# Kernel tuning notes

Hardware: AMD Instinct MI355X
Metric: run time of the kernel (lower is better)

The kernel has to match this reference:

```python
import jax, jax.numpy as jnp
import numpy as np
import math

D_MODEL = 1024
NUM_HEADS = 16
HEAD_DIM = D_MODEL // NUM_HEADS


def setup_inputs() -> dict:
    key = jax.random.key(0)
    ks = jax.random.split(key, 9)
    B, T = 4, 2048
    s = 1.0 / math.sqrt(D_MODEL)
    return {
        "x": jax.random.normal(ks[0], (B, T, D_MODEL), dtype=jnp.float32),
        "Wq": jax.random.normal(ks[1], (D_MODEL, D_MODEL), dtype=jnp.float32) * s,
        "bq": jnp.zeros((D_MODEL,), dtype=jnp.float32),
        "Wk": jax.random.normal(ks[2], (D_MODEL, D_MODEL), dtype=jnp.float32) * s,
        "bk": jnp.zeros((D_MODEL,), dtype=jnp.float32),
        "Wv": jax.random.normal(ks[3], (D_MODEL, D_MODEL), dtype=jnp.float32) * s,
        "bv": jnp.zeros((D_MODEL,), dtype=jnp.float32),
        "Wo": jax.random.normal(ks[4], (D_MODEL, D_MODEL), dtype=jnp.float32) * s,
        "bo": jnp.zeros((D_MODEL,), dtype=jnp.float32),
    }


def reference(x, Wq, bq, Wk, bk, Wv, bv, Wo, bo):
    # x: [B, T, D]. Weights stored as [in, out] (torch Linear weight transposed).
    B, T, D = x.shape
    H, Hd = NUM_HEADS, HEAD_DIM

    def heads(w, b):
        # [B,T,D] -> [B,H,T,Hd]
        return (x @ w + b).reshape(B, T, H, Hd).transpose(0, 2, 1, 3)

    q = heads(Wq, bq)
    k = heads(Wk, bk)
    v = heads(Wv, bv)

    scores = jnp.einsum("bhqd,bhkd->bhqk", q, k) / math.sqrt(Hd)
    attn = jax.nn.softmax(scores, axis=-1)  # dropout is identity in eval mode
    ctx = jnp.einsum("bhqk,bhkd->bhqd", attn, v)
    ctx = ctx.transpose(0, 2, 1, 3).reshape(B, T, D)
    return ctx @ Wo + bo
```

## Files before the change

kernel.cpp:

```cpp
#include <hip/hip_runtime.h>
#include <hip/hip_bf16.h>

#define D_MODEL 1024
#define NHEADS  16
#define HD      64
#define BATCH   4
#define SEQ     2048
#define MROWS   (BATCH*SEQ)

typedef __attribute__((ext_vector_type(8))) short bf16x8;
typedef __attribute__((ext_vector_type(4))) float f32x4;
typedef __attribute__((ext_vector_type(16))) float f32x16;
typedef __attribute__((ext_vector_type(2))) float f32x2;
typedef __attribute__((ext_vector_type(4))) unsigned int u32x4;
typedef __attribute__((ext_vector_type(2))) unsigned int u32x2;
#define MFMA16(a,b,c) __builtin_amdgcn_mfma_f32_16x16x32_bf16(a,b,c,0,0,0)
#define MFMA32(a,b,c) __builtin_amdgcn_mfma_f32_32x32x16_bf16(a,b,c,0,0,0)

__device__ __forceinline__ short f2bf(float f) {
    __hip_bfloat16 h = __float2bfloat16(f);
    return *reinterpret_cast<short*>(&h);
}
__device__ __forceinline__ unsigned cvtpk(float a, float b) {
    unsigned r; asm("v_cvt_pk_bf16_f32 %0, %1, %2" : "=v"(r) : "v"(a), "v"(b)); return r;
}
__device__ __forceinline__ float fexp2(float x) {
    float r; asm("v_exp_f32 %0, %1" : "=v"(r) : "v"(x)); return r;
}
__device__ __forceinline__ f32x2 pkadd(f32x2 a, f32x2 b) {
    f32x2 d; asm("v_pk_add_f32 %0, %1, %2" : "=v"(d) : "v"(a), "v"(b)); return d;
}
#define SH2(V,I) __builtin_shufflevector(V, V, I, (I)+1)

typedef const __attribute__((address_space(1))) unsigned char* gas_t;
typedef __attribute__((address_space(3))) unsigned char* las_t;
#define GLD16(gp, lp) __builtin_amdgcn_global_load_lds((gas_t)(gp), (las_t)(lp), 16, 0, 0)

__global__ __launch_bounds__(256) void prep(
    const float* __restrict__ x,
    const float* __restrict__ Wq, const float* __restrict__ Wk,
    const float* __restrict__ Wv, const float* __restrict__ Wo,
    short* __restrict__ xb,
    short* __restrict__ WqT, short* __restrict__ WkT,
    short* __restrict__ WvT, short* __restrict__ WoT)
{
    __shared__ float tile[64][65];
    const int bid = blockIdx.x;
    const int t = threadIdx.x;
    if (bid < 4096) {
        const size_t i = ((size_t)bid * 256 + t) * 8;
        float4 a = *reinterpret_cast<const float4*>(&x[i]);
        float4 b = *reinterpret_cast<const float4*>(&x[i + 4]);
        bf16x8 v;
        v[0]=f2bf(a.x); v[1]=f2bf(a.y); v[2]=f2bf(a.z); v[3]=f2bf(a.w);
        v[4]=f2bf(b.x); v[5]=f2bf(b.y); v[6]=f2bf(b.z); v[7]=f2bf(b.w);
        *reinterpret_cast<bf16x8*>(&xb[i]) = v;
        return;
    }
    const int tt = bid - 4096;
    const int w = tt >> 8;
    const int tl = tt & 255;
    const int bn = (tl & 15) * 64, bk = (tl >> 4) * 64;
    const float* W = (w==0)?Wq:(w==1)?Wk:(w==2)?Wv:Wo;
    short* out     = (w==0)?WqT:(w==1)?WkT:(w==2)?WvT:WoT;
    const int r = t >> 2, c0 = (t & 3) * 16;
    #pragma unroll
    for (int i = 0; i < 16; i += 4) {
        float4 v = *reinterpret_cast<const float4*>(&W[(size_t)(bk + r) * D_MODEL + bn + c0 + i]);
        tile[r][c0+i] = v.x; tile[r][c0+i+1] = v.y; tile[r][c0+i+2] = v.z; tile[r][c0+i+3] = v.w;
    }
    __syncthreads();
    bf16x8 H0, H1;
    #pragma unroll
    for (int i = 0; i < 8; i++) { H0[i] = f2bf(tile[c0 + i][r]); H1[i] = f2bf(tile[c0 + 8 + i][r]); }
    short* hp = &out[(size_t)(bn + r) * D_MODEL + bk + c0];
    *reinterpret_cast<bf16x8*>(hp) = H0;
    *reinterpret_cast<bf16x8*>(hp + 8) = H1;
}

__global__ __launch_bounds__(256) void gemm_qkv(
    const short* __restrict__ A,
    const short* __restrict__ WqT, const short* __restrict__ WkT, const short* __restrict__ WvT,
    const float* __restrict__ bq, const float* __restrict__ bk, const float* __restrict__ bv,
    short* __restrict__ qo, short* __restrict__ ko, short* __restrict__ vo,
    const float qscale)
{
    __shared__ short As[3][128 * 32];
    __shared__ short Bs[3][128 * 32];
    const int tid = threadIdx.x, wave = tid >> 6, lane = tid & 63;
    const int g = lane >> 4, li = lane & 15;
    const int lin = blockIdx.x + blockIdx.y * 24;
    const int swz = (lin & 7) * 192 + (lin >> 3);
    const int bx = swz % 24, by = swz / 24;
    const int which = bx >> 3;
    const int bm = by * 128, bn = (bx & 7) * 128;
    const int wr = wave >> 1, wc = wave & 1;
    const int lrow = lane >> 2, lcol = (lane & 3) * 8;

    const short* BT = (which == 0) ? WqT : (which == 1) ? WkT : WvT;
    const float* bias = (which == 0) ? bq : (which == 1) ? bk : bv;
    short* out = (which == 0) ? qo : (which == 1) ? ko : vo;
    const float scale = (which == 0) ? qscale : 1.0f;

    f32x4 acc[4][4];
    #pragma unroll
    for (int i = 0; i < 4; i++)
        #pragma unroll
        for (int j = 0; j < 4; j++)
            #pragma unroll
            for (int r = 0; r < 4; r++) acc[i][j][r] = 0.f;

#define STAGEG(KS, BUF) do { \
        const int k0_ = (KS) * 32; \
        _Pragma("unroll") \
        for (int c = 0; c < 2; c++) { \
            const int ch = wave + c * 4; \
            const int row = ch * 16 + lrow; \
            GLD16(&A [(size_t)(bm + row) * D_MODEL + k0_ + lcol], &As[BUF][ch * 512]); \
            GLD16(&BT[(size_t)(bn + row) * D_MODEL + k0_ + lcol], &Bs[BUF][ch * 512]); \
        } \
    } while (0)

    STAGEG(0, 0);
    STAGEG(1, 1);

    const int NSTEP = D_MODEL / 32;
    for (int ks = 0; ks < NSTEP; ks++) {
        const int cur = ks % 3;
        if (ks + 2 < NSTEP) {
            STAGEG(ks + 2, (ks + 2) % 3);
            asm volatile("s_waitcnt vmcnt(8)" ::: "memory");
        } else if (ks + 1 < NSTEP) {
            asm volatile("s_waitcnt vmcnt(4)" ::: "memory");
        } else {
            asm volatile("s_waitcnt vmcnt(0)" ::: "memory");
        }
        __builtin_amdgcn_s_barrier();
        __builtin_amdgcn_sched_barrier(0);

        bf16x8 af[4], bfr[4];
        #pragma unroll
        for (int mi = 0; mi < 4; mi++) af[mi]  = *reinterpret_cast<const bf16x8*>(&As[cur][(wr * 64 + mi * 16 + li) * 32 + g * 8]);
        #pragma unroll
        for (int ni = 0; ni < 4; ni++) bfr[ni] = *reinterpret_cast<const bf16x8*>(&Bs[cur][(wc * 64 + ni * 16 + li) * 32 + g * 8]);
        #pragma unroll
        for (int mi = 0; mi < 4; mi++)
            #pragma unroll
            for (int ni = 0; ni < 4; ni++)
                acc[mi][ni] = MFMA16(af[mi], bfr[ni], acc[mi][ni]);
        __builtin_amdgcn_s_barrier();
    }
#undef STAGEG

    #pragma unroll
    for (int mi = 0; mi < 4; mi++) {
        #pragma unroll
        for (int r = 0; r < 4; r++) {
            const int m = bm + wr * 64 + mi * 16 + g * 4 + r;
            const int b = m >> 11, t = m & (SEQ - 1);
            #pragma unroll
            for (int ni = 0; ni < 4; ni++) {
                const int n = bn + wc * 64 + ni * 16 + li;
                const float val = (acc[mi][ni][r] + bias[n]) * scale;
                const int h = n >> 6, hd = n & 63;
                if (which != 2) out[((size_t)((b * NHEADS + h) * SEQ + t)) * HD + hd] = f2bf(val);
                else            out[((size_t)((b * NHEADS + h) * HD + hd)) * SEQ + t] = f2bf(val);
            }
        }
    }
}

__global__ __launch_bounds__(256) void gemm_wo(
    const short* __restrict__ A, const short* __restrict__ BT,
    const float* __restrict__ bias, float* __restrict__ out)
{
    __shared__ short As[3][128 * 32];
    __shared__ short Bs[3][128 * 32];
    const int tid = threadIdx.x, wave = tid >> 6, lane = tid & 63;
    const int g = lane >> 4, li = lane & 15;
    const int lin = blockIdx.x + blockIdx.y * 8;
    const int swz = (lin & 7) * 64 + (lin >> 3);
    const int bm = (swz >> 3) * 128, bn = (swz & 7) * 128;
    const int wr = wave >> 1, wc = wave & 1;
    const int lrow = lane >> 2, lcol = (lane & 3) * 8;

    f32x4 acc[4][4];
    #pragma unroll
    for (int i = 0; i < 4; i++)
        #pragma unroll
        for (int j = 0; j < 4; j++)
            #pragma unroll
            for (int r = 0; r < 4; r++) acc[i][j][r] = 0.f;

#define STAGEG(KS, BUF) do { \
        const int k0_ = (KS) * 32; \
        _Pragma("unroll") \
        for (int c = 0; c < 2; c++) { \
            const int ch = wave + c * 4; \
            const int row = ch * 16 + lrow; \
            GLD16(&A [(size_t)(bm + row) * D_MODEL + k0_ + lcol], &As[BUF][ch * 512]); \
            GLD16(&BT[(size_t)(bn + row) * D_MODEL + k0_ + lcol], &Bs[BUF][ch * 512]); \
        } \
    } while (0)

    STAGEG(0, 0);
    STAGEG(1, 1);

    const int NSTEP = D_MODEL / 32;
    for (int ks = 0; ks < NSTEP; ks++) {
        const int cur = ks % 3;
        if (ks + 2 < NSTEP) {
            STAGEG(ks + 2, (ks + 2) % 3);
            asm volatile("s_waitcnt vmcnt(8)" ::: "memory");
        } else if (ks + 1 < NSTEP) {
            asm volatile("s_waitcnt vmcnt(4)" ::: "memory");
        } else {
            asm volatile("s_waitcnt vmcnt(0)" ::: "memory");
        }
        __builtin_amdgcn_s_barrier();
        __builtin_amdgcn_sched_barrier(0);

        bf16x8 af[4], bfr[4];
        #pragma unroll
        for (int mi = 0; mi < 4; mi++) af[mi]  = *reinterpret_cast<const bf16x8*>(&As[cur][(wr * 64 + mi * 16 + li) * 32 + g * 8]);
        #pragma unroll
        for (int ni = 0; ni < 4; ni++) bfr[ni] = *reinterpret_cast<const bf16x8*>(&Bs[cur][(wc * 64 + ni * 16 + li) * 32 + g * 8]);
        #pragma unroll
        for (int mi = 0; mi < 4; mi++)
            #pragma unroll
            for (int ni = 0; ni < 4; ni++)
                acc[mi][ni] = MFMA16(af[mi], bfr[ni], acc[mi][ni]);
        __builtin_amdgcn_s_barrier();
    }
#undef STAGEG

    #pragma unroll
    for (int mi = 0; mi < 4; mi++) {
        #pragma unroll
        for (int r = 0; r < 4; r++) {
            const int m = bm + wr * 64 + mi * 16 + g * 4 + r;
            #pragma unroll
            for (int ni = 0; ni < 4; ni++) {
                const int n = bn + wc * 64 + ni * 16 + li;
                out[(size_t)m * D_MODEL + n] = acc[mi][ni][r] + bias[n];
            }
        }
    }
}

__global__ __launch_bounds__(256) void attn_mfma(
    const short* __restrict__ q, const short* __restrict__ k,
    const short* __restrict__ vT, short* __restrict__ ch)
{
    __shared__ short Ks[3][64 * 64];
    __shared__ short Vs[3][64 * 64];

    const int bh = blockIdx.x;
    const int b  = bh >> 4, h = bh & (NHEADS - 1);
    const int qt = blockIdx.y;
    const int tid = threadIdx.x;
    const int wave = tid >> 6, lane = tid & 63;
    const int ql = lane & 31;
    const int hi = lane >> 5;
    const int qand7 = ql & 7;

    const short* qp = q + ((size_t)bh * SEQ + qt * 128 + wave * 32 + ql) * HD;
    const bf16x8 qf0 = *reinterpret_cast<const bf16x8*>(qp + 0  + hi * 8);
    const bf16x8 qf1 = *reinterpret_cast<const bf16x8*>(qp + 16 + hi * 8);
    const bf16x8 qf2 = *reinterpret_cast<const bf16x8*>(qp + 32 + hi * 8);
    const bf16x8 qf3 = *reinterpret_cast<const bf16x8*>(qp + 48 + hi * 8);

    f32x16 o0, o1, Z;
    #pragma unroll
    for (int i = 0; i < 16; i++) { o0[i] = 0.f; o1[i] = 0.f; Z[i] = 0.f; }
    float lR = 0.f;

    const short* kbase = k  + (size_t)bh * SEQ * HD;
    const short* vbase = vT + (size_t)bh * HD * SEQ;

    const int srow = lane >> 3;
    const int gsl  = (lane & 7) ^ srow;
    const int q0 = wave * 2, q1 = wave * 2 + 1;

#define STAGE(T, BUF) do { \
        const short* kg_ = kbase + (size_t)(T) * 64 * HD; \
        const short* vg_ = vbase + (size_t)(T) * 64; \
        GLD16(kg_ + (q0 * 8 + srow) * HD + gsl * 8, &Ks[BUF][q0 * 512]); \
        GLD16(kg_ + (q1 * 8 + srow) * HD + gsl * 8, &Ks[BUF][q1 * 512]); \
        GLD16(vg_ + (size_t)(q0 * 8 + srow) * SEQ + gsl * 8, &Vs[BUF][q0 * 512]); \
        GLD16(vg_ + (size_t)(q1 * 8 + srow) * SEQ + gsl * 8, &Vs[BUF][q1 * 512]); \
    } while (0)

    STAGE(0, 0);
    STAGE(1, 1);

    const int NT = SEQ / 64;
    for (int kt = 0; kt < NT; kt++) {
        const int cur = kt % 3;
        if (kt + 2 < NT) {
            STAGE(kt + 2, (kt + 2) % 3);
            asm volatile("s_waitcnt vmcnt(8)" ::: "memory");
        } else if (kt + 1 < NT) {
            asm volatile("s_waitcnt vmcnt(4)" ::: "memory");
        } else {
            asm volatile("s_waitcnt vmcnt(0)" ::: "memory");
        }
        __builtin_amdgcn_s_barrier();
        __builtin_amdgcn_sched_barrier(0);

        const short* Kb = Ks[cur];
        const short* Vb = Vs[cur];

        f32x16 s0, s1;
        __builtin_amdgcn_s_setprio(1);
#define QK_STEP(DC, QF, C0, C1) do { \
            const int ksl = (((DC) * 2 + hi) ^ qand7) * 8; \
            const bf16x8 ka0 = *reinterpret_cast<const bf16x8*>(&Kb[ql * 64 + ksl]); \
            const bf16x8 ka1 = *reinterpret_cast<const bf16x8*>(&Kb[(32 + ql) * 64 + ksl]); \
            s0 = MFMA32(ka0, QF, C0); \
            s1 = MFMA32(ka1, QF, C1); \
        } while (0)
        QK_STEP(0, qf0, Z, Z);
        QK_STEP(1, qf1, s0, s1);
        QK_STEP(2, qf2, s0, s1);
        QK_STEP(3, qf3, s0, s1);
#undef QK_STEP
        __builtin_amdgcn_s_setprio(0);

        #pragma unroll
        for (int i = 0; i < 16; i++) s0[i] = fexp2(s0[i]);
        #pragma unroll
        for (int i = 0; i < 16; i++) s1[i] = fexp2(s1[i]);
        {
            f32x2 p0 = pkadd(SH2(s0, 0), SH2(s0, 2));
            f32x2 p1 = pkadd(SH2(s0, 4), SH2(s0, 6));
            f32x2 p2 = pkadd(SH2(s0, 8), SH2(s0, 10));
            f32x2 p3 = pkadd(SH2(s0, 12), SH2(s0, 14));
            f32x2 p4 = pkadd(SH2(s1, 0), SH2(s1, 2));
            f32x2 p5 = pkadd(SH2(s1, 4), SH2(s1, 6));
            f32x2 p6 = pkadd(SH2(s1, 8), SH2(s1, 10));
            f32x2 p7 = pkadd(SH2(s1, 12), SH2(s1, 14));
            p0 = pkadd(p0, p1); p2 = pkadd(p2, p3);
            p4 = pkadd(p4, p5); p6 = pkadd(p6, p7);
            p0 = pkadd(p0, p2); p4 = pkadd(p4, p6);
            p0 = pkadd(p0, p4);
            float sum = p0[0] + p0[1];
            sum += __shfl_xor(sum, 32);
            lR += sum;
        }

        __builtin_amdgcn_s_setprio(1);
#define PV_STEP(KB, SS, B) do { \
            const unsigned a0 = cvtpk(SS[(B) + 0], SS[(B) + 1]); \
            const unsigned a1 = cvtpk(SS[(B) + 2], SS[(B) + 3]); \
            const unsigned a2 = cvtpk(SS[(B) + 4], SS[(B) + 5]); \
            const unsigned a3 = cvtpk(SS[(B) + 6], SS[(B) + 7]); \
            const u32x2 r02 = __builtin_amdgcn_permlane32_swap(a0, a2, false, false); \
            const u32x2 r13 = __builtin_amdgcn_permlane32_swap(a1, a3, false, false); \
            u32x4 wv; \
            wv[0] = r02[0]; wv[1] = r13[0]; wv[2] = r02[1]; wv[3] = r13[1]; \
            const bf16x8 pf = __builtin_bit_cast(bf16x8, wv); \
            const int vsl = (((KB) * 2 + hi) ^ qand7) * 8; \
            const bf16x8 vf0 = *reinterpret_cast<const bf16x8*>(&Vb[ql * 64 + vsl]); \
            const bf16x8 vf1 = *reinterpret_cast<const bf16x8*>(&Vb[(32 + ql) * 64 + vsl]); \
            o0 = MFMA32(vf0, pf, o0); \
            o1 = MFMA32(vf1, pf, o1); \
        } while (0)
        PV_STEP(0, s0, 0); PV_STEP(1, s0, 8); PV_STEP(2, s1, 0); PV_STEP(3, s1, 8);
#undef PV_STEP
        __builtin_amdgcn_s_setprio(0);

        __builtin_amdgcn_s_barrier();
    }
#undef STAGE

    const float inv = 1.0f / lR;
    const int t = qt * 128 + wave * 32 + ql;
    const size_t base = ((size_t)(b * SEQ + t)) * D_MODEL + h * HD;
    #pragma unroll
    for (int blk = 0; blk < 4; blk++) {
        uint2 w0, w1;
        w0.x = cvtpk(o0[4*blk + 0] * inv, o0[4*blk + 1] * inv);
        w0.y = cvtpk(o0[4*blk + 2] * inv, o0[4*blk + 3] * inv);
        w1.x = cvtpk(o1[4*blk + 0] * inv, o1[4*blk + 1] * inv);
        w1.y = cvtpk(o1[4*blk + 2] * inv, o1[4*blk + 3] * inv);
        *reinterpret_cast<uint2*>(&ch[base + 8*blk + 4*hi])      = w0;
        *reinterpret_cast<uint2*>(&ch[base + 32 + 8*blk + 4*hi]) = w1;
    }
}

extern "C" void kernel_launch(void* const* d_in, const int* in_sizes, int n_in,
                              void* d_out, int out_size, void* d_ws, size_t ws_size,
                              hipStream_t stream) {
    const float* x  = (const float*)d_in[0];
    const float* Wq = (const float*)d_in[1];
    const float* bq = (const float*)d_in[2];
    const float* Wk = (const float*)d_in[3];
    const float* bk = (const float*)d_in[4];
    const float* Wv = (const float*)d_in[5];
    const float* bv = (const float*)d_in[6];
    const float* Wo = (const float*)d_in[7];
    const float* bo = (const float*)d_in[8];

    const size_t S1 = (size_t)MROWS * D_MODEL;
    const size_t SW = (size_t)D_MODEL * D_MODEL;
    short* xb  = (short*)d_ws;
    short* qb  = xb + S1;
    short* kb  = qb + S1;
    short* vb  = kb + S1;
    short* chb = vb + S1;
    short* WqT = chb + S1;
    short* WkT = WqT + SW;
    short* WvT = WkT + SW;
    short* WoT = WvT + SW;

    prep<<<5120, 256, 0, stream>>>(x, Wq, Wk, Wv, Wo, xb, WqT, WkT, WvT, WoT);

    const float QSCALE = 0.125f * 1.4426950408889634f;
    gemm_qkv<<<dim3(24, 64), 256, 0, stream>>>(xb, WqT, WkT, WvT, bq, bk, bv,
                                               qb, kb, vb, QSCALE);
    attn_mfma<<<dim3(BATCH * NHEADS, SEQ / 128), 256, 0, stream>>>(qb, kb, vb, chb);
    gemm_wo<<<dim3(8, 64), 256, 0, stream>>>(chb, WoT, bo, (float*)d_out);
}
```

Baseline: 220.7 us.

## Preswizzle LDS tiles into MFMA fragment order, drop trailing barrier, software-pipeline PV

Global-to-LDS staging now writes each 16- or 32-row chunk directly in the per-lane MFMA fragment layout, so every fragment read becomes a contiguous lane*8 offset with no XOR swizzle. The prefetch for stage k+2 moves after the top-of-loop barrier, which lets the second barrier per iteration be removed from all three kernels. In attention, the PV MFMAs for tile k are deferred into iteration k+1 and overlap with QK, with V fragments and packed probabilities carried across iterations in registers. This adds register pressure and depends on the single remaining barrier to avoid overwriting buffers that are still being read.

```diff
diff --git a/kernel.cpp b/kernel.cpp
--- a/kernel.cpp
+++ b/kernel.cpp
@@ -95,7 +95,10 @@
     const int which = bx >> 3;
     const int bm = by * 128, bn = (bx & 7) * 128;
     const int wr = wave >> 1, wc = wave & 1;
-    const int lrow = lane >> 2, lcol = (lane & 3) * 8;
+    const int lb = lane * 8;
+    const int arow0 = wave * 16 + li;
+    const int arow1 = (wave + 4) * 16 + li;
+    const int acol  = g * 8;
 
     const short* BT = (which == 0) ? WqT : (which == 1) ? WkT : WvT;
     const float* bias = (which == 0) ? bq : (which == 1) ? bk : bv;
@@ -112,13 +115,10 @@
 
 #define STAGEG(KS, BUF) do { \
         const int k0_ = (KS) * 32; \
-        _Pragma("unroll") \
-        for (int c = 0; c < 2; c++) { \
-            const int ch = wave + c * 4; \
-            const int row = ch * 16 + lrow; \
-            GLD16(&A [(size_t)(bm + row) * D_MODEL + k0_ + lcol], &As[BUF][ch * 512]); \
-            GLD16(&BT[(size_t)(bn + row) * D_MODEL + k0_ + lcol], &Bs[BUF][ch * 512]); \
-        } \
+        GLD16(&A [(size_t)(bm + arow0) * D_MODEL + k0_ + acol], &As[BUF][wave * 512]); \
+        GLD16(&A [(size_t)(bm + arow1) * D_MODEL + k0_ + acol], &As[BUF][(wave + 4) * 512]); \
+        GLD16(&BT[(size_t)(bn + arow0) * D_MODEL + k0_ + acol], &Bs[BUF][wave * 512]); \
+        GLD16(&BT[(size_t)(bn + arow1) * D_MODEL + k0_ + acol], &Bs[BUF][(wave + 4) * 512]); \
     } while (0)
 
     STAGEG(0, 0);
@@ -127,28 +127,22 @@
     const int NSTEP = D_MODEL / 32;
     for (int ks = 0; ks < NSTEP; ks++) {
         const int cur = ks % 3;
-        if (ks + 2 < NSTEP) {
-            STAGEG(ks + 2, (ks + 2) % 3);
-            asm volatile("s_waitcnt vmcnt(8)" ::: "memory");
-        } else if (ks + 1 < NSTEP) {
-            asm volatile("s_waitcnt vmcnt(4)" ::: "memory");
-        } else {
-            asm volatile("s_waitcnt vmcnt(0)" ::: "memory");
-        }
+        if (ks + 1 < NSTEP) asm volatile("s_waitcnt vmcnt(4)" ::: "memory");
+        else                asm volatile("s_waitcnt vmcnt(0)" ::: "memory");
         __builtin_amdgcn_s_barrier();
         __builtin_amdgcn_sched_barrier(0);
+        if (ks + 2 < NSTEP) STAGEG(ks + 2, (ks + 2) % 3);
 
         bf16x8 af[4], bfr[4];
         #pragma unroll
-        for (int mi = 0; mi < 4; mi++) af[mi]  = *reinterpret_cast<const bf16x8*>(&As[cur][(wr * 64 + mi * 16 + li) * 32 + g * 8]);
-        #pragma unroll
-        for (int ni = 0; ni < 4; ni++) bfr[ni] = *reinterpret_cast<const bf16x8*>(&Bs[cur][(wc * 64 + ni * 16 + li) * 32 + g * 8]);
+        for (int mi = 0; mi < 4; mi++) af[mi]  = *reinterpret_cast<const bf16x8*>(&As[cur][(wr * 4 + mi) * 512 + lb]);
+        #pragma unroll
+        for (int ni = 0; ni < 4; ni++) bfr[ni] = *reinterpret_cast<const bf16x8*>(&Bs[cur][(wc * 4 + ni) * 512 + lb]);
         #pragma unroll
         for (int mi = 0; mi < 4; mi++)
             #pragma unroll
             for (int ni = 0; ni < 4; ni++)
                 acc[mi][ni] = MFMA16(af[mi], bfr[ni], acc[mi][ni]);
-        __builtin_amdgcn_s_barrier();
     }
 #undef STAGEG
 
@@ -182,7 +176,10 @@
     const int swz = (lin & 7) * 64 + (lin >> 3);
     const int bm = (swz >> 3) * 128, bn = (swz & 7) * 128;
     const int wr = wave >> 1, wc = wave & 1;
-    const int lrow = lane >> 2, lcol = (lane & 3) * 8;
+    const int lb = lane * 8;
+    const int arow0 = wave * 16 + li;
+    const int arow1 = (wave + 4) * 16 + li;
+    const int acol  = g * 8;
 
     f32x4 acc[4][4];
     #pragma unroll
@@ -194,13 +191,10 @@
 
 #define STAGEG(KS, BUF) do { \
         const int k0_ = (KS) * 32; \
-        _Pragma("unroll") \
-        for (int c = 0; c < 2; c++) { \
-            const int ch = wave + c * 4; \
-            const int row = ch * 16 + lrow; \
-            GLD16(&A [(size_t)(bm + row) * D_MODEL + k0_ + lcol], &As[BUF][ch * 512]); \
-            GLD16(&BT[(size_t)(bn + row) * D_MODEL + k0_ + lcol], &Bs[BUF][ch * 512]); \
-        } \
+        GLD16(&A [(size_t)(bm + arow0) * D_MODEL + k0_ + acol], &As[BUF][wave * 512]); \
+        GLD16(&A [(size_t)(bm + arow1) * D_MODEL + k0_ + acol], &As[BUF][(wave + 4) * 512]); \
+        GLD16(&BT[(size_t)(bn + arow0) * D_MODEL + k0_ + acol], &Bs[BUF][wave * 512]); \
+        GLD16(&BT[(size_t)(bn + arow1) * D_MODEL + k0_ + acol], &Bs[BUF][(wave + 4) * 512]); \
     } while (0)
 
     STAGEG(0, 0);
@@ -209,28 +203,22 @@
     const int NSTEP = D_MODEL / 32;
     for (int ks = 0; ks < NSTEP; ks++) {
         const int cur = ks % 3;
-        if (ks + 2 < NSTEP) {
-            STAGEG(ks + 2, (ks + 2) % 3);
-            asm volatile("s_waitcnt vmcnt(8)" ::: "memory");
-        } else if (ks + 1 < NSTEP) {
-            asm volatile("s_waitcnt vmcnt(4)" ::: "memory");
-        } else {
-            asm volatile("s_waitcnt vmcnt(0)" ::: "memory");
-        }
+        if (ks + 1 < NSTEP) asm volatile("s_waitcnt vmcnt(4)" ::: "memory");
+        else                asm volatile("s_waitcnt vmcnt(0)" ::: "memory");
         __builtin_amdgcn_s_barrier();
         __builtin_amdgcn_sched_barrier(0);
+        if (ks + 2 < NSTEP) STAGEG(ks + 2, (ks + 2) % 3);
 
         bf16x8 af[4], bfr[4];
         #pragma unroll
-        for (int mi = 0; mi < 4; mi++) af[mi]  = *reinterpret_cast<const bf16x8*>(&As[cur][(wr * 64 + mi * 16 + li) * 32 + g * 8]);
-        #pragma unroll
-        for (int ni = 0; ni < 4; ni++) bfr[ni] = *reinterpret_cast<const bf16x8*>(&Bs[cur][(wc * 64 + ni * 16 + li) * 32 + g * 8]);
+        for (int mi = 0; mi < 4; mi++) af[mi]  = *reinterpret_cast<const bf16x8*>(&As[cur][(wr * 4 + mi) * 512 + lb]);
+        #pragma unroll
+        for (int ni = 0; ni < 4; ni++) bfr[ni] = *reinterpret_cast<const bf16x8*>(&Bs[cur][(wc * 4 + ni) * 512 + lb]);
         #pragma unroll
         for (int mi = 0; mi < 4; mi++)
             #pragma unroll
             for (int ni = 0; ni < 4; ni++)
                 acc[mi][ni] = MFMA16(af[mi], bfr[ni], acc[mi][ni]);
-        __builtin_amdgcn_s_barrier();
     }
 #undef STAGEG
 
@@ -262,7 +250,7 @@
     const int wave = tid >> 6, lane = tid & 63;
     const int ql = lane & 31;
     const int hi = lane >> 5;
-    const int qand7 = ql & 7;
+    const int lb = lane * 8;
 
     const short* qp = q + ((size_t)bh * SEQ + qt * 128 + wave * 32 + ql) * HD;
     const bf16x8 qf0 = *reinterpret_cast<const bf16x8*>(qp + 0  + hi * 8);
@@ -278,45 +266,43 @@
     const short* kbase = k  + (size_t)bh * SEQ * HD;
     const short* vbase = vT + (size_t)bh * HD * SEQ;
 
-    const int srow = lane >> 3;
-    const int gsl  = (lane & 7) ^ srow;
-    const int q0 = wave * 2, q1 = wave * 2 + 1;
+    const int r0 = wave * 2, r1 = wave * 2 + 1;
+    const int kof0 = ((r0 & 1) * 32 + ql) * HD + (r0 >> 1) * 16 + hi * 8;
+    const int kof1 = ((r1 & 1) * 32 + ql) * HD + (r1 >> 1) * 16 + hi * 8;
+    const size_t vof0 = (size_t)((r0 & 1) * 32 + ql) * SEQ + (r0 >> 1) * 16 + hi * 8;
+    const size_t vof1 = (size_t)((r1 & 1) * 32 + ql) * SEQ + (r1 >> 1) * 16 + hi * 8;
 
 #define STAGE(T, BUF) do { \
         const short* kg_ = kbase + (size_t)(T) * 64 * HD; \
         const short* vg_ = vbase + (size_t)(T) * 64; \
-        GLD16(kg_ + (q0 * 8 + srow) * HD + gsl * 8, &Ks[BUF][q0 * 512]); \
-        GLD16(kg_ + (q1 * 8 + srow) * HD + gsl * 8, &Ks[BUF][q1 * 512]); \
-        GLD16(vg_ + (size_t)(q0 * 8 + srow) * SEQ + gsl * 8, &Vs[BUF][q0 * 512]); \
-        GLD16(vg_ + (size_t)(q1 * 8 + srow) * SEQ + gsl * 8, &Vs[BUF][q1 * 512]); \
+        GLD16(kg_ + kof0, &Ks[BUF][r0 * 512]); \
+        GLD16(kg_ + kof1, &Ks[BUF][r1 * 512]); \
+        GLD16(vg_ + vof0, &Vs[BUF][r0 * 512]); \
+        GLD16(vg_ + vof1, &Vs[BUF][r1 * 512]); \
     } while (0)
+
+    u32x4 pp[4];
+    bf16x8 vr0[4], vr1[4];
 
     STAGE(0, 0);
     STAGE(1, 1);
 
     const int NT = SEQ / 64;
     for (int kt = 0; kt < NT; kt++) {
-        const int cur = kt % 3;
-        if (kt + 2 < NT) {
-            STAGE(kt + 2, (kt + 2) % 3);
-            asm volatile("s_waitcnt vmcnt(8)" ::: "memory");
-        } else if (kt + 1 < NT) {
-            asm volatile("s_waitcnt vmcnt(4)" ::: "memory");
-        } else {
-            asm volatile("s_waitcnt vmcnt(0)" ::: "memory");
-        }
+        if (kt + 1 < NT) asm volatile("s_waitcnt vmcnt(4)" ::: "memory");
+        else             asm volatile("s_waitcnt vmcnt(0)" ::: "memory");
         __builtin_amdgcn_s_barrier();
         __builtin_amdgcn_sched_barrier(0);
-
-        const short* Kb = Ks[cur];
-        const short* Vb = Vs[cur];
+        if (kt + 2 < NT) STAGE(kt + 2, (kt + 2) % 3);
+
+        const short* Kb = Ks[kt % 3];
+        const short* Vb = Vs[kt % 3];
 
         f32x16 s0, s1;
         __builtin_amdgcn_s_setprio(1);
 #define QK_STEP(DC, QF, C0, C1) do { \
-            const int ksl = (((DC) * 2 + hi) ^ qand7) * 8; \
-            const bf16x8 ka0 = *reinterpret_cast<const bf16x8*>(&Kb[ql * 64 + ksl]); \
-            const bf16x8 ka1 = *reinterpret_cast<const bf16x8*>(&Kb[(32 + ql) * 64 + ksl]); \
+            const bf16x8 ka0 = *reinterpret_cast<const bf16x8*>(&Kb[((DC) * 2 + 0) * 512 + lb]); \
+            const bf16x8 ka1 = *reinterpret_cast<const bf16x8*>(&Kb[((DC) * 2 + 1) * 512 + lb]); \
             s0 = MFMA32(ka0, QF, C0); \
             s1 = MFMA32(ka1, QF, C1); \
         } while (0)
@@ -325,6 +311,20 @@
         QK_STEP(2, qf2, s0, s1);
         QK_STEP(3, qf3, s0, s1);
 #undef QK_STEP
+
+        if (kt > 0) {
+            #pragma unroll
+            for (int KB = 0; KB < 4; KB++) {
+                const bf16x8 pf = __builtin_bit_cast(bf16x8, pp[KB]);
+                o0 = MFMA32(vr0[KB], pf, o0);
+                o1 = MFMA32(vr1[KB], pf, o1);
+            }
+        }
+        #pragma unroll
+        for (int KB = 0; KB < 4; KB++) {
+            vr0[KB] = *reinterpret_cast<const bf16x8*>(&Vb[(KB * 2 + 0) * 512 + lb]);
+            vr1[KB] = *reinterpret_cast<const bf16x8*>(&Vb[(KB * 2 + 1) * 512 + lb]);
+        }
         __builtin_amdgcn_s_setprio(0);
 
         #pragma unroll
@@ -349,30 +349,29 @@
             lR += sum;
         }
 
-        __builtin_amdgcn_s_setprio(1);
-#define PV_STEP(KB, SS, B) do { \
+#define PACK(KB, SS, B) do { \
             const unsigned a0 = cvtpk(SS[(B) + 0], SS[(B) + 1]); \
             const unsigned a1 = cvtpk(SS[(B) + 2], SS[(B) + 3]); \
             const unsigned a2 = cvtpk(SS[(B) + 4], SS[(B) + 5]); \
             const unsigned a3 = cvtpk(SS[(B) + 6], SS[(B) + 7]); \
             const u32x2 r02 = __builtin_amdgcn_permlane32_swap(a0, a2, false, false); \
             const u32x2 r13 = __builtin_amdgcn_permlane32_swap(a1, a3, false, false); \
-            u32x4 wv; \
-            wv[0] = r02[0]; wv[1] = r13[0]; wv[2] = r02[1]; wv[3] = r13[1]; \
-            const bf16x8 pf = __builtin_bit_cast(bf16x8, wv); \
-            const int vsl = (((KB) * 2 + hi) ^ qand7) * 8; \
-            const bf16x8 vf0 = *reinterpret_cast<const bf16x8*>(&Vb[ql * 64 + vsl]); \
-            const bf16x8 vf1 = *reinterpret_cast<const bf16x8*>(&Vb[(32 + ql) * 64 + vsl]); \
-            o0 = MFMA32(vf0, pf, o0); \
-            o1 = MFMA32(vf1, pf, o1); \
+            pp[KB][0] = r02[0]; pp[KB][1] = r13[0]; pp[KB][2] = r02[1]; pp[KB][3] = r13[1]; \
         } while (0)
-        PV_STEP(0, s0, 0); PV_STEP(1, s0, 8); PV_STEP(2, s1, 0); PV_STEP(3, s1, 8);
-#undef PV_STEP
-        __builtin_amdgcn_s_setprio(0);
-
-        __builtin_amdgcn_s_barrier();
+        PACK(0, s0, 0); PACK(1, s0, 8); PACK(2, s1, 0); PACK(3, s1, 8);
+#undef PACK
+
+        asm volatile("s_waitcnt lgkmcnt(0)" ::: "memory");
+        __builtin_amdgcn_sched_barrier(0);
     }
 #undef STAGE
+
+    #pragma unroll
+    for (int KB = 0; KB < 4; KB++) {
+        const bf16x8 pf = __builtin_bit_cast(bf16x8, pp[KB]);
+        o0 = MFMA32(vr0[KB], pf, o0);
+        o1 = MFMA32(vr1[KB], pf, o1);
+    }
 
     const float inv = 1.0f / lR;
     const int t = qt * 128 + wave * 32 + ql;
```

Measured after the change: 265.5 us. 1.2x slower.
